# Kernel tuning notes

Hardware: AMD Instinct MI355X
Metric: run time of the kernel (lower is better)

Reference implementation:

```python
import jax, jax.numpy as jnp
import numpy as np

N_NODES = 50000


def setup_inputs() -> dict:
    key = jax.random.key(0)
    ks = jax.random.split(key, 6)
    d_in, d_out = 256, 256
    n_edges = 1_600_000
    x = jax.random.normal(ks[0], (N_NODES, d_in), dtype=jnp.float32)
    edge_index = jax.random.randint(ks[1], (2, n_edges), 0, N_NODES, dtype=jnp.int64)
    edge_attr = jax.random.normal(ks[2], (n_edges, 16), dtype=jnp.float32)  # unused by forward
    W1 = jax.random.normal(ks[3], (d_in, d_out), dtype=jnp.float32) * (1.0 / np.sqrt(d_in))
    b1 = jnp.zeros((d_out,), dtype=jnp.float32)
    W2 = jax.random.normal(ks[4], (d_out, d_out), dtype=jnp.float32) * (1.0 / np.sqrt(d_out))
    b2 = jnp.zeros((d_out,), dtype=jnp.float32)
    eps = jnp.zeros((1,), dtype=jnp.float32)  # train_eps=True, init 0
    return {"x": x, "edge_index": edge_index, "edge_attr": edge_attr,
            "W1": W1, "b1": b1, "W2": W2, "b2": b2, "eps": eps}


def reference(x, edge_index, edge_attr, W1, b1, W2, b2, eps):
    src, dst = edge_index[0], edge_index[1]
    # sum aggregation: agg[i] = sum_{(j->i) in E} x[j]
    agg = jax.ops.segment_sum(x[src], dst, num_segments=N_NODES)  # [N, d_in]
    h = (1.0 + eps[0]) * x + agg
    # MLP: Linear -> ReLU -> (dropout=0) -> Linear
    h = jax.nn.relu(h @ W1 + b1)
    out = h @ W2 + b2
    return out
```

## Files before the change

### kernel.cpp

```cpp
#include <hip/hip_runtime.h>
#include <stdint.h>

#define NODES 50000
#define D 256
#define MP 50048
#define NBUCK 196
#define CAP 10240
#define EPB 4096

typedef short bf16x8 __attribute__((ext_vector_type(8)));
typedef float f32x4 __attribute__((ext_vector_type(4)));

__device__ inline unsigned short f2b(float f) {
    unsigned int u = __float_as_uint(f);
    unsigned int r = (u + 0x7fffu + ((u >> 16) & 1u)) >> 16;
    return (unsigned short)r;
}

__device__ inline bool ei_is64(const int* ei) {
    return (ei[1] | ei[3] | ei[5] | ei[7]) == 0;
}
__device__ inline int ei_get(const int* __restrict__ ei, long long pos, bool is64) {
    return is64 ? ei[2 * pos] : ei[(int)pos];
}

__global__ __launch_bounds__(256) void cast_x_kernel(const float* __restrict__ x,
                                                     unsigned short* __restrict__ xb) {
    int t = blockIdx.x * 256 + threadIdx.x;
    float4 v = ((const float4*)x)[t];
    unsigned int lo = (unsigned int)f2b(v.x) | ((unsigned int)f2b(v.y) << 16);
    unsigned int hi = (unsigned int)f2b(v.z) | ((unsigned int)f2b(v.w) << 16);
    ((uint2*)xb)[t] = make_uint2(lo, hi);
}

__global__ __launch_bounds__(256) void zero_kernel(int* __restrict__ p, int n) {
    int t = blockIdx.x * 256 + threadIdx.x;
    if (t < n) p[t] = 0;
}

__global__ __launch_bounds__(256) void pack_w_kernel(const float* __restrict__ W1,
                                                     const float* __restrict__ W2,
                                                     unsigned short* __restrict__ P1,
                                                     unsigned short* __restrict__ P2) {
    int t = blockIdx.x * 256 + threadIdx.x;
    const float* W = (t < 8192) ? W1 : W2;
    unsigned short* P = (t < 8192) ? P1 : P2;
    int u = t & 8191;
    int lane = u & 63, nt = (u >> 6) & 15, s = u >> 10;
    int q = lane >> 4, n = nt * 16 + (lane & 15);
    int kbase = s * 32 + q * 8;
#pragma unroll
    for (int j = 0; j < 8; j++) P[u * 8 + j] = f2b(W[(kbase + j) * D + n]);
}

__global__ __launch_bounds__(256) void partA_kernel(const int* __restrict__ ei, int E,
                                                    int* __restrict__ bcnt,
                                                    unsigned int* __restrict__ ebufT) {
    __shared__ int cnt[256];
    __shared__ int gbase[256];
    __shared__ int lcur[256];
    bool is64 = ei_is64(ei);
    int tid = threadIdx.x;
    cnt[tid] = 0;
    lcur[tid] = 0;
    __syncthreads();
    long long blockStart = (long long)blockIdx.x * EPB;
    unsigned int w[16];
    int bk[16];
#pragma unroll
    for (int r = 0; r < 16; r++) {
        long long e = blockStart + r * 256 + tid;
        bk[r] = -1;
        if (e < E) {
            int src = ei_get(ei, e, is64);
            int dst = ei_get(ei, (long long)E + e, is64);
            bk[r] = dst >> 8;
            w[r] = ((unsigned int)(dst & 255) << 16) | (unsigned int)src;
            atomicAdd(&cnt[bk[r]], 1);
        }
    }
    __syncthreads();
    if (tid < NBUCK && cnt[tid] > 0) gbase[tid] = atomicAdd(&bcnt[tid], cnt[tid]);
    __syncthreads();
#pragma unroll
    for (int r = 0; r < 16; r++) {
        if (bk[r] >= 0) {
            int p = atomicAdd(&lcur[bk[r]], 1);
            ebufT[(size_t)bk[r] * CAP + gbase[bk[r]] + p] = w[r];
        }
    }
}

__global__ __launch_bounds__(256) void bscan_kernel(const int* __restrict__ bcnt,
                                                    int* __restrict__ bstart,
                                                    int* __restrict__ offs, int E) {
    __shared__ int buf[256];
    int tid = threadIdx.x;
    int v = (tid < NBUCK) ? bcnt[tid] : 0;
    buf[tid] = v;
    __syncthreads();
    for (int off = 1; off < 256; off <<= 1) {
        int xv = (tid >= off) ? buf[tid - off] : 0;
        __syncthreads();
        buf[tid] += xv;
        __syncthreads();
    }
    if (tid < NBUCK) bstart[tid] = buf[tid] - v;
    if (tid == 0) offs[NODES] = E;
}

__global__ __launch_bounds__(256) void partB_kernel(const int* __restrict__ bcnt,
                                                    const int* __restrict__ bstart,
                                                    const unsigned int* __restrict__ ebufT,
                                                    int* __restrict__ offs,
                                                    int* __restrict__ ebuf) {
    __shared__ int ncnt[256];
    __shared__ int ncur[256];
    int b = blockIdx.x, tid = threadIdx.x;
    int n = bcnt[b];
    int base = bstart[b];
    ncnt[tid] = 0;
    __syncthreads();
    const unsigned int* reg = ebufT + (size_t)b * CAP;
    for (int i = tid; i < n; i += 256) {
        unsigned int w = reg[i];
        atomicAdd(&ncnt[w >> 16], 1);
    }
    __syncthreads();
    int v = ncnt[tid];
    ncur[tid] = v;
    __syncthreads();
    for (int off = 1; off < 256; off <<= 1) {
        int xv = (tid >= off) ? ncur[tid - off] : 0;
        __syncthreads();
        ncur[tid] += xv;
        __syncthreads();
    }
    int excl = ncur[tid] - v;
    int node = b * 256 + tid;
    if (node < NODES) offs[node] = base + excl;
    __syncthreads();
    ncur[tid] = excl;
    __syncthreads();
    for (int i = tid; i < n; i += 256) {
        unsigned int w = reg[i];
        int p = atomicAdd(&ncur[w >> 16], 1);
        ebuf[base + p] = (int)(w & 0xffffu);
    }
}

__global__ __launch_bounds__(256) void agg_kernel(const unsigned short* __restrict__ xb,
                                                  const int* __restrict__ offs,
                                                  const int* __restrict__ ebuf,
                                                  const float* __restrict__ eps,
                                                  unsigned short* __restrict__ h0) {
    int wv = (blockIdx.x * 256 + threadIdx.x) >> 6;
    int lane = threadIdx.x & 63;
    if (wv >= NODES) return;
    float scale = 1.0f + eps[0];
    uint2 v = ((const uint2*)(xb + (size_t)wv * D))[lane];
    float a0 = __uint_as_float(v.x << 16) * scale;
    float a1 = __uint_as_float(v.x & 0xffff0000u) * scale;
    float a2 = __uint_as_float(v.y << 16) * scale;
    float a3 = __uint_as_float(v.y & 0xffff0000u) * scale;
    int beg = offs[wv], end = offs[wv + 1];
    for (int base = beg; base < end; base += 64) {
        int id = 0;
        if (base + lane < end) id = ebuf[base + lane];
        int m = min(64, end - base);
        for (int j = 0; j < m; j++) {
            int s = __shfl(id, j);
            uint2 w = *(const uint2*)(xb + (size_t)s * D + lane * 4);
            a0 += __uint_as_float(w.x << 16);
            a1 += __uint_as_float(w.x & 0xffff0000u);
            a2 += __uint_as_float(w.y << 16);
            a3 += __uint_as_float(w.y & 0xffff0000u);
        }
    }
    unsigned int lo = (unsigned int)f2b(a0) | ((unsigned int)f2b(a1) << 16);
    unsigned int hi = (unsigned int)f2b(a2) | ((unsigned int)f2b(a3) << 16);
    ((uint2*)(h0 + (size_t)wv * D))[lane] = make_uint2(lo, hi);
}

template <int RELU, int OUTBF16>
__global__ __launch_bounds__(256) void gemm_kernel(const unsigned short* __restrict__ A,
                                                   const unsigned short* __restrict__ Bp,
                                                   const float* __restrict__ bias,
                                                   void* __restrict__ out, int Mvalid) {
    int wv = threadIdx.x >> 6;
    int lane = threadIdx.x & 63;
    int quad = lane >> 4, l16 = lane & 15;
    int mBase = blockIdx.x * 64;
    f32x4 acc[4][4] = {};
    const bf16x8* Bv = (const bf16x8*)Bp;
#pragma unroll
    for (int ks = 0; ks < 8; ks++) {
        bf16x8 a[4], b[4];
#pragma unroll
        for (int mi = 0; mi < 4; mi++) {
            int row = mBase + mi * 16 + l16;
            a[mi] = *(const bf16x8*)(A + (size_t)row * D + ks * 32 + quad * 8);
        }
#pragma unroll
        for (int ni = 0; ni < 4; ni++) {
            int nt = wv * 4 + ni;
            b[ni] = Bv[(ks * 16 + nt) * 64 + lane];
        }
#pragma unroll
        for (int mi = 0; mi < 4; mi++)
#pragma unroll
            for (int ni = 0; ni < 4; ni++)
                acc[mi][ni] =
                    __builtin_amdgcn_mfma_f32_16x16x32_bf16(a[mi], b[ni], acc[mi][ni], 0, 0, 0);
    }
#pragma unroll
    for (int mi = 0; mi < 4; mi++) {
#pragma unroll
        for (int ni = 0; ni < 4; ni++) {
            int col = wv * 64 + ni * 16 + l16;
            float bs = bias[col];
#pragma unroll
            for (int r = 0; r < 4; r++) {
                int row = mBase + mi * 16 + quad * 4 + r;
                if (row < Mvalid) {
                    float v = acc[mi][ni][r] + bs;
                    if (RELU) v = fmaxf(v, 0.0f);
                    if (OUTBF16)
                        ((unsigned short*)out)[(size_t)row * D + col] = f2b(v);
                    else
                        ((float*)out)[(size_t)row * D + col] = v;
                }
            }
        }
    }
}

extern "C" void kernel_launch(void* const* d_in, const int* in_sizes, int n_in,
                              void* d_out, int out_size, void* d_ws, size_t ws_size,
                              hipStream_t stream) {
    const float* x = (const float*)d_in[0];
    const int* ei = (const int*)d_in[1];
    const float* W1 = (const float*)d_in[3];
    const float* b1 = (const float*)d_in[4];
    const float* W2 = (const float*)d_in[5];
    const float* b2 = (const float*)d_in[6];
    const float* eps = (const float*)d_in[7];
    int E = in_sizes[1] / 2;

    char* p = (char*)d_ws;
    auto alloc = [&](size_t bytes) {
        char* r = p;
        p += (bytes + 255) & ~(size_t)255;
        return r;
    };
    unsigned short* xb = (unsigned short*)alloc((size_t)MP * D * 2);
    unsigned short* h0 = (unsigned short*)alloc((size_t)MP * D * 2);
    unsigned short* P1 = (unsigned short*)alloc(8192 * 8 * 2);
    unsigned short* P2 = (unsigned short*)alloc(8192 * 8 * 2);
    int* bcnt = (int*)alloc((size_t)NBUCK * 4);
    int* bstart = (int*)alloc((size_t)(NBUCK + 1) * 4);
    int* offs = (int*)alloc((size_t)(NODES + 1) * 4);
    int* ebuf = (int*)alloc((size_t)E * 4);
    unsigned int* ebufT = (unsigned int*)alloc((size_t)NBUCK * CAP * 4);
    unsigned short* h1 = xb;

    cast_x_kernel<<<NODES * D / 4 / 256, 256, 0, stream>>>(x, xb);
    zero_kernel<<<1, 256, 0, stream>>>(bcnt, NBUCK);
    pack_w_kernel<<<64, 256, 0, stream>>>(W1, W2, P1, P2);
    partA_kernel<<<(E + EPB - 1) / EPB, 256, 0, stream>>>(ei, E, bcnt, ebufT);
    bscan_kernel<<<1, 256, 0, stream>>>(bcnt, bstart, offs, E);
    partB_kernel<<<NBUCK, 256, 0, stream>>>(bcnt, bstart, ebufT, offs, ebuf);
    agg_kernel<<<(NODES + 3) / 4, 256, 0, stream>>>(xb, offs, ebuf, eps, h0);
    gemm_kernel<1, 1><<<MP / 64, 256, 0, stream>>>(h0, P1, b1, h1, NODES);
    gemm_kernel<0, 0><<<MP / 64, 256, 0, stream>>>(h1, P2, b2, d_out, NODES);
}
```

Baseline: 416.1 us.

## Fuse two MLP GEMMs via LDS, widen aggregation gathers, fold zeroing into cast

The two GEMM launches become one kernel. It keeps the ReLU hidden tile in padded shared memory, which removes the h1 global write and readback. The aggregation kernel now has each half-wave gather a different neighbor with 16-byte loads, using two accumulator sets to expose more memory parallelism, and the halves are reduced with a cross-lane shuffle. The bucket-count zeroing moves into the cast kernel to drop one launch. The costs are more registers in aggregation and extra LDS use in the fused GEMM.

```diff
diff --git a/kernel.cpp b/kernel.cpp
--- a/kernel.cpp
+++ b/kernel.cpp
@@ -7,6 +7,7 @@
 #define NBUCK 196
 #define CAP 10240
 #define EPB 4096
+#define HS_LD 264
 
 typedef short bf16x8 __attribute__((ext_vector_type(8)));
 typedef float f32x4 __attribute__((ext_vector_type(4)));
@@ -25,17 +26,14 @@
 }
 
 __global__ __launch_bounds__(256) void cast_x_kernel(const float* __restrict__ x,
-                                                     unsigned short* __restrict__ xb) {
+                                                     unsigned short* __restrict__ xb,
+                                                     int* __restrict__ bcnt) {
+    if (blockIdx.x == 0 && threadIdx.x < NBUCK) bcnt[threadIdx.x] = 0;
     int t = blockIdx.x * 256 + threadIdx.x;
     float4 v = ((const float4*)x)[t];
     unsigned int lo = (unsigned int)f2b(v.x) | ((unsigned int)f2b(v.y) << 16);
     unsigned int hi = (unsigned int)f2b(v.z) | ((unsigned int)f2b(v.w) << 16);
     ((uint2*)xb)[t] = make_uint2(lo, hi);
-}
-
-__global__ __launch_bounds__(256) void zero_kernel(int* __restrict__ p, int n) {
-    int t = blockIdx.x * 256 + threadIdx.x;
-    if (t < n) p[t] = 0;
 }
 
 __global__ __launch_bounds__(256) void pack_w_kernel(const float* __restrict__ W1,
@@ -149,6 +147,17 @@
     }
 }
 
+__device__ inline void upk_add(uint4 w, float* a) {
+    a[0] += __uint_as_float(w.x << 16);
+    a[1] += __uint_as_float(w.x & 0xffff0000u);
+    a[2] += __uint_as_float(w.y << 16);
+    a[3] += __uint_as_float(w.y & 0xffff0000u);
+    a[4] += __uint_as_float(w.z << 16);
+    a[5] += __uint_as_float(w.z & 0xffff0000u);
+    a[6] += __uint_as_float(w.w << 16);
+    a[7] += __uint_as_float(w.w & 0xffff0000u);
+}
+
 __global__ __launch_bounds__(256) void agg_kernel(const unsigned short* __restrict__ xb,
                                                   const int* __restrict__ offs,
                                                   const int* __restrict__ ebuf,
@@ -157,82 +166,139 @@
     int wv = (blockIdx.x * 256 + threadIdx.x) >> 6;
     int lane = threadIdx.x & 63;
     if (wv >= NODES) return;
-    float scale = 1.0f + eps[0];
-    uint2 v = ((const uint2*)(xb + (size_t)wv * D))[lane];
-    float a0 = __uint_as_float(v.x << 16) * scale;
-    float a1 = __uint_as_float(v.x & 0xffff0000u) * scale;
-    float a2 = __uint_as_float(v.y << 16) * scale;
-    float a3 = __uint_as_float(v.y & 0xffff0000u) * scale;
+    int half = lane >> 5;
+    int l32 = lane & 31;
+    float aA[8] = {0, 0, 0, 0, 0, 0, 0, 0};
+    float aB[8] = {0, 0, 0, 0, 0, 0, 0, 0};
     int beg = offs[wv], end = offs[wv + 1];
     for (int base = beg; base < end; base += 64) {
         int id = 0;
         if (base + lane < end) id = ebuf[base + lane];
         int m = min(64, end - base);
-        for (int j = 0; j < m; j++) {
-            int s = __shfl(id, j);
-            uint2 w = *(const uint2*)(xb + (size_t)s * D + lane * 4);
-            a0 += __uint_as_float(w.x << 16);
-            a1 += __uint_as_float(w.x & 0xffff0000u);
-            a2 += __uint_as_float(w.y << 16);
-            a3 += __uint_as_float(w.y & 0xffff0000u);
-        }
-    }
-    unsigned int lo = (unsigned int)f2b(a0) | ((unsigned int)f2b(a1) << 16);
-    unsigned int hi = (unsigned int)f2b(a2) | ((unsigned int)f2b(a3) << 16);
-    ((uint2*)(h0 + (size_t)wv * D))[lane] = make_uint2(lo, hi);
-}
-
-template <int RELU, int OUTBF16>
-__global__ __launch_bounds__(256) void gemm_kernel(const unsigned short* __restrict__ A,
-                                                   const unsigned short* __restrict__ Bp,
-                                                   const float* __restrict__ bias,
-                                                   void* __restrict__ out, int Mvalid) {
+        int j = 0;
+        for (; j + 4 <= m; j += 4) {
+            int sA = __shfl(id, j + half);
+            int sB = __shfl(id, j + 2 + half);
+            uint4 wA = *(const uint4*)(xb + (size_t)sA * D + l32 * 8);
+            uint4 wB = *(const uint4*)(xb + (size_t)sB * D + l32 * 8);
+            upk_add(wA, aA);
+            upk_add(wB, aB);
+        }
+        for (; j + 2 <= m; j += 2) {
+            int sA = __shfl(id, j + half);
+            uint4 wA = *(const uint4*)(xb + (size_t)sA * D + l32 * 8);
+            upk_add(wA, aA);
+        }
+        if (j < m) {
+            int sA = __shfl(id, j);
+            if (half == 0) {
+                uint4 wA = *(const uint4*)(xb + (size_t)sA * D + l32 * 8);
+                upk_add(wA, aA);
+            }
+        }
+    }
+    float a[8];
+#pragma unroll
+    for (int i = 0; i < 8; i++) {
+        a[i] = aA[i] + aB[i];
+        a[i] += __shfl_xor(a[i], 32);
+    }
+    if (half == 0) {
+        float scale = 1.0f + eps[0];
+        uint4 v = *(const uint4*)(xb + (size_t)wv * D + l32 * 8);
+        a[0] += scale * __uint_as_float(v.x << 16);
+        a[1] += scale * __uint_as_float(v.x & 0xffff0000u);
+        a[2] += scale * __uint_as_float(v.y << 16);
+        a[3] += scale * __uint_as_float(v.y & 0xffff0000u);
+        a[4] += scale * __uint_as_float(v.z << 16);
+        a[5] += scale * __uint_as_float(v.z & 0xffff0000u);
+        a[6] += scale * __uint_as_float(v.w << 16);
+        a[7] += scale * __uint_as_float(v.w & 0xffff0000u);
+        uint4 o;
+        o.x = (unsigned int)f2b(a[0]) | ((unsigned int)f2b(a[1]) << 16);
+        o.y = (unsigned int)f2b(a[2]) | ((unsigned int)f2b(a[3]) << 16);
+        o.z = (unsigned int)f2b(a[4]) | ((unsigned int)f2b(a[5]) << 16);
+        o.w = (unsigned int)f2b(a[6]) | ((unsigned int)f2b(a[7]) << 16);
+        ((uint4*)(h0 + (size_t)wv * D))[l32] = o;
+    }
+}
+
+__global__ __launch_bounds__(256) void gemm_fused_kernel(const unsigned short* __restrict__ A,
+                                                         const unsigned short* __restrict__ P1,
+                                                         const float* __restrict__ b1,
+                                                         const unsigned short* __restrict__ P2,
+                                                         const float* __restrict__ b2,
+                                                         float* __restrict__ out, int Mvalid) {
+    __shared__ unsigned short hs[64 * HS_LD];
     int wv = threadIdx.x >> 6;
     int lane = threadIdx.x & 63;
     int quad = lane >> 4, l16 = lane & 15;
     int mBase = blockIdx.x * 64;
+    const bf16x8* B1v = (const bf16x8*)P1;
+    const bf16x8* B2v = (const bf16x8*)P2;
+
+    {
+        f32x4 acc[4][4] = {};
+#pragma unroll
+        for (int ks = 0; ks < 8; ks++) {
+            bf16x8 af[4], bf[4];
+#pragma unroll
+            for (int mi = 0; mi < 4; mi++) {
+                int row = mBase + mi * 16 + l16;
+                af[mi] = *(const bf16x8*)(A + (size_t)row * D + ks * 32 + quad * 8);
+            }
+#pragma unroll
+            for (int ni = 0; ni < 4; ni++) bf[ni] = B1v[(ks * 16 + wv * 4 + ni) * 64 + lane];
+#pragma unroll
+            for (int mi = 0; mi < 4; mi++)
+#pragma unroll
+                for (int ni = 0; ni < 4; ni++)
+                    acc[mi][ni] = __builtin_amdgcn_mfma_f32_16x16x32_bf16(af[mi], bf[ni],
+                                                                          acc[mi][ni], 0, 0, 0);
+        }
+#pragma unroll
+        for (int mi = 0; mi < 4; mi++)
+#pragma unroll
+            for (int ni = 0; ni < 4; ni++) {
+                int col = wv * 64 + ni * 16 + l16;
+                float bs = b1[col];
+#pragma unroll
+                for (int r = 0; r < 4; r++) {
+                    int rl = mi * 16 + quad * 4 + r;
+                    hs[rl * HS_LD + col] = f2b(fmaxf(acc[mi][ni][r] + bs, 0.0f));
+                }
+            }
+    }
+    __syncthreads();
+
     f32x4 acc[4][4] = {};
-    const bf16x8* Bv = (const bf16x8*)Bp;
 #pragma unroll
     for (int ks = 0; ks < 8; ks++) {
-        bf16x8 a[4], b[4];
-#pragma unroll
-        for (int mi = 0; mi < 4; mi++) {
-            int row = mBase + mi * 16 + l16;
-            a[mi] = *(const bf16x8*)(A + (size_t)row * D + ks * 32 + quad * 8);
-        }
-#pragma unroll
-        for (int ni = 0; ni < 4; ni++) {
-            int nt = wv * 4 + ni;
-            b[ni] = Bv[(ks * 16 + nt) * 64 + lane];
-        }
+        bf16x8 af[4], bf[4];
+#pragma unroll
+        for (int mi = 0; mi < 4; mi++)
+            af[mi] = *(const bf16x8*)(hs + (mi * 16 + l16) * HS_LD + ks * 32 + quad * 8);
+#pragma unroll
+        for (int ni = 0; ni < 4; ni++) bf[ni] = B2v[(ks * 16 + wv * 4 + ni) * 64 + lane];
 #pragma unroll
         for (int mi = 0; mi < 4; mi++)
 #pragma unroll
             for (int ni = 0; ni < 4; ni++)
                 acc[mi][ni] =
-                    __builtin_amdgcn_mfma_f32_16x16x32_bf16(a[mi], b[ni], acc[mi][ni], 0, 0, 0);
-    }
-#pragma unroll
-    for (int mi = 0; mi < 4; mi++) {
+                    __builtin_amdgcn_mfma_f32_16x16x32_bf16(af[mi], bf[ni], acc[mi][ni], 0, 0, 0);
+    }
+#pragma unroll
+    for (int mi = 0; mi < 4; mi++)
 #pragma unroll
         for (int ni = 0; ni < 4; ni++) {
             int col = wv * 64 + ni * 16 + l16;
-            float bs = bias[col];
+            float bs = b2[col];
 #pragma unroll
             for (int r = 0; r < 4; r++) {
                 int row = mBase + mi * 16 + quad * 4 + r;
-                if (row < Mvalid) {
-                    float v = acc[mi][ni][r] + bs;
-                    if (RELU) v = fmaxf(v, 0.0f);
-                    if (OUTBF16)
-                        ((unsigned short*)out)[(size_t)row * D + col] = f2b(v);
-                    else
-                        ((float*)out)[(size_t)row * D + col] = v;
-                }
+                if (row < Mvalid) out[(size_t)row * D + col] = acc[mi][ni][r] + bs;
             }
         }
-    }
 }
 
 extern "C" void kernel_launch(void* const* d_in, const int* in_sizes, int n_in,
@@ -262,15 +328,12 @@
     int* offs = (int*)alloc((size_t)(NODES + 1) * 4);
     int* ebuf = (int*)alloc((size_t)E * 4);
     unsigned int* ebufT = (unsigned int*)alloc((size_t)NBUCK * CAP * 4);
-    unsigned short* h1 = xb;
-
-    cast_x_kernel<<<NODES * D / 4 / 256, 256, 0, stream>>>(x, xb);
-    zero_kernel<<<1, 256, 0, stream>>>(bcnt, NBUCK);
+
+    cast_x_kernel<<<NODES * D / 4 / 256, 256, 0, stream>>>(x, xb, bcnt);
     pack_w_kernel<<<64, 256, 0, stream>>>(W1, W2, P1, P2);
     partA_kernel<<<(E + EPB - 1) / EPB, 256, 0, stream>>>(ei, E, bcnt, ebufT);
     bscan_kernel<<<1, 256, 0, stream>>>(bcnt, bstart, offs, E);
     partB_kernel<<<NBUCK, 256, 0, stream>>>(bcnt, bstart, ebufT, offs, ebuf);
     agg_kernel<<<(NODES + 3) / 4, 256, 0, stream>>>(xb, offs, ebuf, eps, h0);
-    gemm_kernel<1, 1><<<MP / 64, 256, 0, stream>>>(h0, P1, b1, h1, NODES);
-    gemm_kernel<0, 0><<<MP / 64, 256, 0, stream>>>(h1, P2, b2, d_out, NODES);
-}
+    gemm_fused_kernel<<<MP / 64, 256, 0, stream>>>(h0, P1, b1, P2, b2, (float*)d_out, NODES);
+}
```

Result: faster. 379.7 us (-8.7%).
